# Kernel optimization log

Measured on AMD Instinct MI355X. Metric: run time of the kernel, lower is better.

Reference implementation:

```python
import jax, jax.numpy as jnp
import numpy as np

B, LQ, LF, NW, NFR, E, D, V = 4, 128, 64, 2, 8, 128, 128, 64


def _project(x, W, b):
    # torch Emb_Projection('linear'): Linear then zero-row mask
    y = x @ W + b
    m = 1.0 - jnp.all(y == 0, axis=-1, keepdims=True).astype(y.dtype)
    return y * m


def setup_inputs() -> dict:
    key = jax.random.key(0)
    ks = jax.random.split(key, 12)
    s = lambda k, shape, fan: jax.random.normal(k, shape, jnp.float32) / np.sqrt(fan)
    return {
        "query": jax.random.normal(ks[0], (B, LQ, E), jnp.float32),
        "fragment": jax.random.normal(ks[1], (B, NW, NFR, LF, E), jnp.float32),
        "query_mask": jnp.ones((B, LQ), jnp.float32),
        "fragment_mask": jnp.ones((B, NW, NFR, LF), jnp.float32),
        # learned params (stored [in, out]; torch Linear is x @ W.T with W [out,in])
        "proj_W": s(ks[2], (E, D), E),
        "proj_b": jnp.zeros((D,), jnp.float32),
        "self_att_W": s(ks[3], (NW, D), D),   # n_way Linear(D,1,bias=False)
        "q_att_W": s(ks[4], (D, V), D),
        "f_att_W": s(ks[5], (D, V), D),
        "qf_att_W": s(ks[6], (D, V), D),
        "gate_w": s(ks[7], (V,), V),          # value_gate: Linear(V,1,bias=False)
        "val_w": s(ks[8], (V,), V),           # value_att:  Linear(V,1,bias=False)
    }


def reference(query, fragment, query_mask, fragment_mask, proj_W, proj_b,
              self_att_W, q_att_W, f_att_W, qf_att_W, gate_w, val_w):
    query = _project(query, proj_W, proj_b)          # [B,Lq,D]
    fragment = _project(fragment, proj_W, proj_b)    # [B,NW,NFR,Lf,D]

    # (1) fragment self-attention -> frag_code
    logits = jnp.einsum('bwfld,wd->bwfl', fragment, self_att_W)   # per-way Linear(D,1)
    e = jnp.exp(logits) * fragment_mask
    frag_self_att = e / (e.sum(-1, keepdims=True) + 1e-7)          # [B,NW,NFR,Lf]
    frag_code = (fragment * frag_self_att[..., None]).sum(-2)     # [B,NW,NFR,D]

    # (2) query-to-fragment attention
    frag_r = fragment.reshape(fragment.shape[0], -1, fragment.shape[-2], fragment.shape[-1])  # [B,NF,Lf,D]
    qr = query[:, None]                                            # [B,1,Lq,D]
    q_att = qr @ q_att_W                                           # [B,1,Lq,V]
    f_att = frag_r @ f_att_W                                       # [B,NF,Lf,V]
    # large broadcast product [B,NF,Lf,Lq,D] then project to V
    qf = (qr[:, :, None, :, :] * frag_r[:, :, :, None, :]) @ qf_att_W  # [B,NF,Lf,Lq,V]
    qf = q_att[:, :, None] + f_att[:, :, :, None] + qf
    qf = qf.max(axis=-3)                                           # max over Lf -> [B,NF,Lq,V]

    qf_gate = jax.nn.sigmoid(qf @ gate_w) * query_mask[:, None]    # [B,NF,Lq]
    e2 = jnp.exp(qf @ val_w) * query_mask[:, None]
    qf_norm = e2 / (e2.sum(-1, keepdims=True) + 1e-7)              # [B,NF,Lq]

    query_code = (qr * qf_norm[..., None]).sum(axis=2)             # [B,NF,D]
    query_code = query_code.reshape(frag_code.shape)               # [B,NW,NFR,D]
    return frag_code, query_code, frag_self_att, qf_gate, query
```

## Files before the change

kernel.cpp:

```cpp
#include <hip/hip_runtime.h>
#include <hip/hip_bf16.h>

#define B_   4
#define LQ_  128
#define LF_  64
#define NW_  2
#define NFR_ 8
#define E_   128
#define D_   128
#define V_   64
#define NWF_ (NW_*NFR_)
#define NROW_Q (B_*LQ_)
#define NROW_F (B_*NW_*NFR_*LF_)

using bf16 = __hip_bfloat16;
typedef unsigned short u16;
typedef unsigned int   u32;
typedef __attribute__((ext_vector_type(8))) short  bf16x8;
typedef __attribute__((ext_vector_type(4))) float  f32x4;
typedef __attribute__((ext_vector_type(4))) u32    u32x4;

#define WS_QP    0
#define WS_QATT  65536
#define WS_E2    98304
#define WS_FP16  106496
#define WS_W3T   368640
#define WS_WFT   372736
#define WS_PWT   376832
#define WS_QAT   385024

#define OUT_FRAGCODE  0
#define OUT_QUERYCODE 8192
#define OUT_SELFATT   16384
#define OUT_QFGATE    20480
#define OUT_QUERY     28672

__device__ __forceinline__ float us2f(u16 v) { return __uint_as_float((u32)v << 16); }
__device__ __forceinline__ float lo2f(u32 v) { return __uint_as_float(v << 16); }
__device__ __forceinline__ float hi2f(u32 v) { return __uint_as_float(v & 0xffff0000u); }
__device__ __forceinline__ u16 f2b_raw(float f) {
    u32 u = __float_as_uint(f);
    return (u16)((u + 0x7fffu + ((u >> 16) & 1u)) >> 16);
}
__device__ __forceinline__ u32 pk2(float hi, float lo) {
    return __builtin_amdgcn_perm(__float_as_uint(hi), __float_as_uint(lo), 0x07060302u);
}
template<bool BF> __device__ __forceinline__ float LD(const void* p, int i) {
    return BF ? us2f(((const u16*)p)[i]) : ((const float*)p)[i];
}
template<bool BF> __device__ __forceinline__ void ST(void* p, int i, float v) {
    if (BF) ((u16*)p)[i] = f2b_raw(v); else ((float*)p)[i] = v;
}
template<bool BF> __device__ __forceinline__ u16 LDB(const void* p, int i) {
    return BF ? ((const u16*)p)[i] : f2b_raw(((const float*)p)[i]);
}
__device__ __forceinline__ bool is_bf(const void* qmask) {
    return ((const u16*)qmask)[0] == 0x3F80u;
}

template<bool BF>
__device__ __forceinline__ void prep_body(const void* src, u16* dst, u16* stg, int N)
{
    int t = threadIdx.x;
    int st = N + 1, total = 128 * N;
    for (int i = t; i < total; i += 256)
        stg[(i / N) * st + (i % N)] = LDB<BF>(src, i);
    __syncthreads();
    for (int j = t; j < total; j += 256) {
        int n = j >> 7, k = j & 127;
        dst[n * 128 + k] = stg[k * st + n];
    }
}
__global__ __launch_bounds__(256) void k_prep(
    const void* projW, const void* qattW, const void* qfW, const void* fattW,
    const void* qmask, float* ws)
{
    __shared__ u16 stg[128 * 129];
    int bx = blockIdx.x;
    const void* src = (bx == 0) ? projW : (bx == 1) ? qattW : (bx == 2) ? qfW : fattW;
    u16* dst = (u16*)(ws + ((bx == 0) ? WS_PWT : (bx == 1) ? WS_QAT : (bx == 2) ? WS_W3T : WS_WFT));
    int N = (bx == 0) ? 128 : 64;
    if (is_bf(qmask)) prep_body<true >(src, dst, stg, N);
    else              prep_body<false>(src, dst, stg, N);
}

template<bool BF>
__device__ __forceinline__ void proj_body(
    const void* query, const void* fragment, const void* projB,
    float* ws, void* out, u16* s_y)
{
    int r = blockIdx.x, t = threadIdx.x;
    int lane = t & 63, wave = t >> 6, m = lane & 15, quad = lane >> 4;
    bool isq = (r >= 256);
    int base = isq ? (r - 256) * 16 : r * 16;
    const void* x = isq ? query : fragment;
    const u16* pwt = (const u16*)(ws + WS_PWT);

    bf16x8 af[4];
    #pragma unroll
    for (int kt = 0; kt < 4; ++kt) {
        int off = (base + m) * 128 + kt * 32 + quad * 8;
        if (BF) af[kt] = *(const bf16x8*)((const u16*)x + off);
        else {
            f32x4 a = *(const f32x4*)((const float*)x + off);
            f32x4 c = *(const f32x4*)((const float*)x + off + 4);
            u32x4 av;
            av.x = pk2(a.y, a.x); av.y = pk2(a.w, a.z);
            av.z = pk2(c.y, c.x); av.w = pk2(c.w, c.z);
            af[kt] = __builtin_bit_cast(bf16x8, av);
        }
    }
    int nt0 = wave * 2;
    f32x4 acc[2];
    #pragma unroll
    for (int i = 0; i < 2; ++i) {
        float bv = LD<BF>(projB, (nt0 + i) * 16 + m);
        acc[i] = (f32x4){bv, bv, bv, bv};
    }
    #pragma unroll
    for (int kt = 0; kt < 4; ++kt)
        #pragma unroll
        for (int i = 0; i < 2; ++i) {
            bf16x8 bfr = *(const bf16x8*)(pwt + ((nt0 + i) * 16 + m) * 128 + kt * 32 + quad * 8);
            acc[i] = __builtin_amdgcn_mfma_f32_16x16x32_bf16(af[kt], bfr, acc[i], 0, 0, 0);
        }
    if (!isq) {
        u16* fp16 = (u16*)(ws + WS_FP16);
        #pragma unroll
        for (int i = 0; i < 2; ++i)
            #pragma unroll
            for (int rr = 0; rr < 4; ++rr)
                fp16[(size_t)(base + quad * 4 + rr) * 128 + (nt0 + i) * 16 + m] = f2b_raw(acc[i][rr]);
    } else {
        #pragma unroll
        for (int i = 0; i < 2; ++i)
            #pragma unroll
            for (int rr = 0; rr < 4; ++rr) {
                int gr = base + quad * 4 + rr, col = (nt0 + i) * 16 + m;
                float v = acc[i][rr];
                ws[WS_QP + (size_t)gr * 128 + col] = v;
                ST<BF>(out, OUT_QUERY + gr * 128 + col, v);
                s_y[(quad * 4 + rr) * 132 + col] = f2b_raw(v);
            }
        __syncthreads();
        bf16x8 ay[4];
        #pragma unroll
        for (int kt = 0; kt < 4; ++kt)
            ay[kt] = *(const bf16x8*)&s_y[m * 132 + kt * 32 + quad * 8];
        const u16* qat = (const u16*)(ws + WS_QAT);
        f32x4 a2 = (f32x4){0.f, 0.f, 0.f, 0.f};
        #pragma unroll
        for (int kt = 0; kt < 4; ++kt) {
            bf16x8 b2 = *(const bf16x8*)(qat + (wave * 16 + m) * 128 + kt * 32 + quad * 8);
            a2 = __builtin_amdgcn_mfma_f32_16x16x32_bf16(ay[kt], b2, a2, 0, 0, 0);
        }
        #pragma unroll
        for (int rr = 0; rr < 4; ++rr)
            ws[WS_QATT + (size_t)(base + quad * 4 + rr) * 64 + wave * 16 + m] = a2[rr];
    }
}
__global__ __launch_bounds__(256) void k_proj(
    const void* query, const void* fragment, const void* projB, const void* qmask,
    float* ws, void* out)
{
    __shared__ u16 s_y[16 * 132];
    if (is_bf(qmask)) proj_body<true >(query, fragment, projB, ws, out, s_y);
    else              proj_body<false>(query, fragment, projB, ws, out, s_y);
}

template<bool BF>
__device__ __forceinline__ void qf_body(
    const void* saW, const void* fmask, const void* gatew, const void* valw,
    const void* qmask, float* ws, void* out, char* smem)
{
    u16*   s_fp  = (u16*)smem;
    u16*   s_fa  = (u16*)(smem + 16384);
    float* s_saw = (float*)(smem + 34816);
    float* s_att = (float*)(smem + 35328);
    float* s_tmp = (float*)(smem + 35584);

    int t = threadIdx.x, lane = t & 63, wave = t >> 6;
    int bwf = blockIdx.x >> 2, qt2 = blockIdx.x & 3;
    int b = bwf >> 4;
    int m = lane & 15, quad = lane >> 4;
    int lq = wave >> 1, qsub = wave & 1;
    int sk = (m & 7) << 3;

    {
        const u32* src = (const u32*)((const u16*)(ws + WS_FP16)) + (size_t)bwf * 4096;
        u32* d32 = (u32*)s_fp;
        #pragma unroll
        for (int k = 0; k < 16; ++k) {
            int i = t + 512 * k;
            int row = i >> 6, cp = i & 63;
            d32[row * 64 + (cp ^ ((row & 7) << 2))] = src[i];
        }
    }
    const u16* w3t = (const u16*)(ws + WS_W3T);
    bf16x8 w3f[4][4];
    #pragma unroll
    for (int vt = 0; vt < 4; ++vt)
        #pragma unroll
        for (int kt = 0; kt < 4; ++kt)
            w3f[vt][kt] = *(const bf16x8*)(w3t + (vt * 16 + m) * 128 + kt * 32 + quad * 8);
    __syncthreads();

    int lbase = lq * 16;
    if (qsub == 0) {
        const u16* wft = (const u16*)(ws + WS_WFT);
        bf16x8 afk[4];
        #pragma unroll
        for (int kt = 0; kt < 4; ++kt)
            afk[kt] = *(const bf16x8*)&s_fp[(lbase + m) * 128 + ((kt * 32 + quad * 8) ^ sk)];
        #pragma unroll
        for (int vt = 0; vt < 4; ++vt) {
            bf16x8 wf = *(const bf16x8*)(wft + (vt * 16 + m) * 128 + 0 * 32 + quad * 8);
            f32x4 a0 = (f32x4){0.f, 0.f, 0.f, 0.f};
            #pragma unroll
            for (int kt = 0; kt < 4; ++kt) {
                bf16x8 wk = *(const bf16x8*)(wft + (vt * 16 + m) * 128 + kt * 32 + quad * 8);
                a0 = __builtin_amdgcn_mfma_f32_16x16x32_bf16(afk[kt], wk, a0, 0, 0, 0);
                (void)wf;
            }
            #pragma unroll
            for (int r = 0; r < 4; ++r)
                s_fa[(lbase + quad * 4 + r) * 72 + vt * 16 + m] = f2b_raw(a0[r]);
        }
    }
    float qpreg[4][8];
    {
        const float* qprow = ws + WS_QP + (size_t)(b * LQ_ + qt2 * 32 + qsub * 16 + m) * 128;
        #pragma unroll
        for (int kt = 0; kt < 4; ++kt) {
            f32x4 x0 = *(const f32x4*)(qprow + kt * 32 + quad * 8);
            f32x4 x1 = *(const f32x4*)(qprow + kt * 32 + quad * 8 + 4);
            qpreg[kt][0] = x0.x; qpreg[kt][1] = x0.y; qpreg[kt][2] = x0.z; qpreg[kt][3] = x0.w;
            qpreg[kt][4] = x1.x; qpreg[kt][5] = x1.y; qpreg[kt][6] = x1.z; qpreg[kt][7] = x1.w;
        }
    }
    __syncthreads();

    float mx[4][4];
    #pragma unroll
    for (int vt = 0; vt < 4; ++vt)
        #pragma unroll
        for (int r = 0; r < 4; ++r) mx[vt][r] = -1e30f;

    u32x4 fvc[4], fvn[4];
    #pragma unroll
    for (int kt = 0; kt < 4; ++kt)
        fvc[kt] = *(const u32x4*)&s_fp[lbase * 128 + (kt * 32 + quad * 8)];
    #pragma unroll 2
    for (int li = 0; li < 16; ++li) {
        if (li < 15) {
            int l2 = lbase + li + 1;
            #pragma unroll
            for (int kt = 0; kt < 4; ++kt)
                fvn[kt] = *(const u32x4*)&s_fp[l2 * 128 + ((kt * 32 + quad * 8) ^ (((li + 1) & 7) << 3))];
        }
        int l = lbase + li;
        bf16x8 af[4];
        #pragma unroll
        for (int kt = 0; kt < 4; ++kt) {
            u32x4 fv = fvc[kt];
            u32x4 av;
            av.x = pk2(qpreg[kt][1] * hi2f(fv.x), qpreg[kt][0] * lo2f(fv.x));
            av.y = pk2(qpreg[kt][3] * hi2f(fv.y), qpreg[kt][2] * lo2f(fv.y));
            av.z = pk2(qpreg[kt][5] * hi2f(fv.z), qpreg[kt][4] * lo2f(fv.z));
            av.w = pk2(qpreg[kt][7] * hi2f(fv.w), qpreg[kt][6] * lo2f(fv.w));
            af[kt] = __builtin_bit_cast(bf16x8, av);
        }
        #pragma unroll
        for (int vt = 0; vt < 4; ++vt) {
            float fa = us2f(s_fa[l * 72 + vt * 16 + m]);
            f32x4 acc = (f32x4){fa, fa, fa, fa};
            #pragma unroll
            for (int kt = 0; kt < 4; ++kt)
                acc = __builtin_amdgcn_mfma_f32_16x16x32_bf16(af[kt], w3f[vt][kt], acc, 0, 0, 0);
            #pragma unroll
            for (int r = 0; r < 4; ++r) mx[vt][r] = fmaxf(mx[vt][r], acc[r]);
        }
        #pragma unroll
        for (int kt = 0; kt < 4; ++kt) fvc[kt] = fvn[kt];
    }
    __syncthreads();
    #pragma unroll
    for (int vt = 0; vt < 4; ++vt)
        #pragma unroll
        for (int r = 0; r < 4; ++r)
            s_fa[(lq * 32 + qsub * 16 + quad * 4 + r) * 72 + vt * 16 + m] = f2b_raw(mx[vt][r]);
    __syncthreads();

    {
        int q = t >> 4, vg = t & 15;
        int gq = qt2 * 32 + q;
        float gp = 0.f, ep = 0.f;
        #pragma unroll
        for (int jj = 0; jj < 4; ++jj) {
            int v = vg * 4 + jj;
            float mval = -1e30f;
            #pragma unroll
            for (int w = 0; w < 4; ++w)
                mval = fmaxf(mval, us2f(s_fa[(w * 32 + q) * 72 + v]));
            float qf = mval + ws[WS_QATT + (size_t)(b * LQ_ + gq) * 64 + v];
            gp += qf * LD<BF>(gatew, v);
            ep += qf * LD<BF>(valw, v);
        }
        #pragma unroll
        for (int off = 1; off <= 8; off <<= 1) {
            gp += __shfl_xor(gp, off, 64);
            ep += __shfl_xor(ep, off, 64);
        }
        if (vg == 0) {
            float qm = LD<BF>(qmask, b * LQ_ + gq);
            float g = (1.0f / (1.0f + expf(-gp))) * qm;
            ST<BF>(out, OUT_QFGATE + bwf * LQ_ + gq, g);
            ws[WS_E2 + bwf * LQ_ + gq] = expf(ep) * qm;
        }
    }

    if (qt2 == 0) {
        if (t < 128) s_saw[t] = LD<BF>(saW, ((bwf >> 3) & 1) * 128 + t);
        __syncthreads();
        int l = t >> 3, j8 = t & 7;
        int swz = (l & 7) << 3;
        float p = 0.f;
        #pragma unroll
        for (int seg = 0; seg < 2; ++seg) {
            int koff = j8 * 16 + seg * 8;
            u32x4 fv = *(const u32x4*)&s_fp[l * 128 + (koff ^ swz)];
            const float* swp = &s_saw[koff];
            p += lo2f(fv.x) * swp[0] + hi2f(fv.x) * swp[1]
               + lo2f(fv.y) * swp[2] + hi2f(fv.y) * swp[3]
               + lo2f(fv.z) * swp[4] + hi2f(fv.z) * swp[5]
               + lo2f(fv.w) * swp[6] + hi2f(fv.w) * swp[7];
        }
        p += __shfl_xor(p, 1, 64);
        p += __shfl_xor(p, 2, 64);
        p += __shfl_xor(p, 4, 64);
        if (j8 == 0) s_att[l] = expf(p) * LD<BF>(fmask, bwf * LF_ + l);
        __syncthreads();
        if (t < 64) {
            float e = s_att[t], s = e;
            #pragma unroll
            for (int off = 1; off <= 32; off <<= 1) s += __shfl_xor(s, off, 64);
            float nrm = e / (s + 1e-7f);
            s_att[t] = nrm;
            ST<BF>(out, OUT_SELFATT + bwf * LF_ + t, nrm);
        }
        __syncthreads();
        int d = t & 127, grp = t >> 7;
        float fc = 0.f;
        #pragma unroll
        for (int li2 = 0; li2 < 16; ++li2) {
            int l2 = grp * 16 + li2;
            fc += us2f(s_fp[l2 * 128 + (d ^ ((l2 & 7) << 3))]) * s_att[l2];
        }
        s_tmp[grp * 128 + d] = fc;
        __syncthreads();
        if (t < 128)
            ST<BF>(out, OUT_FRAGCODE + bwf * D_ + t,
                   s_tmp[t] + s_tmp[128 + t] + s_tmp[256 + t] + s_tmp[384 + t]);
    }
}
__global__ __launch_bounds__(512) void k_qf(
    const void* saW, const void* fmask, const void* gatew, const void* valw,
    const void* qmask, float* ws, void* out)
{
    __shared__ char smem[37632];
    if (is_bf(qmask)) qf_body<true >(saW, fmask, gatew, valw, qmask, ws, out, smem);
    else              qf_body<false>(saW, fmask, gatew, valw, qmask, ws, out, smem);
}

template<bool BF>
__device__ __forceinline__ void qcode_body(const float* ws, void* out,
                                           float* s_n, float* s_part)
{
    int bwf = blockIdx.x, b = bwf >> 4, t = threadIdx.x;
    float e = ws[WS_E2 + bwf * LQ_ + t];
    float s = e;
    #pragma unroll
    for (int off = 1; off <= 32; off <<= 1) s += __shfl_xor(s, off, 64);
    if ((t & 63) == 0) s_part[t >> 6] = s;
    __syncthreads();
    float tot = s_part[0] + s_part[1] + 1e-7f;
    s_n[t] = e / tot;
    __syncthreads();
    float qc = 0.f;
    #pragma unroll 8
    for (int q = 0; q < LQ_; ++q)
        qc += ws[WS_QP + (size_t)(b * LQ_ + q) * 128 + t] * s_n[q];
    ST<BF>(out, OUT_QUERYCODE + bwf * D_ + t, qc);
}
__global__ __launch_bounds__(128) void k_qcode(const void* qmask, const float* ws, void* out)
{
    __shared__ float s_n[LQ_];
    __shared__ float s_part[2];
    if (is_bf(qmask)) qcode_body<true >(ws, out, s_n, s_part);
    else              qcode_body<false>(ws, out, s_n, s_part);
}

extern "C" void kernel_launch(void* const* d_in, const int* in_sizes, int n_in,
                              void* d_out, int out_size, void* d_ws, size_t ws_size,
                              hipStream_t stream)
{
    const void* query    = d_in[0];
    const void* fragment = d_in[1];
    const void* qmask    = d_in[2];
    const void* fmask    = d_in[3];
    const void* projW    = d_in[4];
    const void* projB    = d_in[5];
    const void* saW      = d_in[6];
    const void* qattW    = d_in[7];
    const void* fattW    = d_in[8];
    const void* qfW      = d_in[9];
    const void* gatew    = d_in[10];
    const void* valw     = d_in[11];
    float* ws = (float*)d_ws;

    hipLaunchKernelGGL(k_prep, dim3(4), dim3(256), 0, stream,
                       projW, qattW, qfW, fattW, qmask, ws);
    hipLaunchKernelGGL(k_proj, dim3(288), dim3(256), 0, stream,
                       query, fragment, projB, qmask, ws, d_out);
    hipLaunchKernelGGL(k_qf, dim3(256), dim3(512), 0, stream,
                       saW, fmask, gatew, valw, qmask, ws, d_out);
    hipLaunchKernelGGL(k_qcode, dim3(B_ * NWF_), dim3(128), 0, stream,
                       qmask, ws, d_out);
}
```

Baseline: 114.2 us.

## Fold weight prep into projection kernel and re-split qf work across more blocks

Removes the separate weight-transpose kernel. The projection kernel now reads projW and qattW directly with strided scalar loads, and two extra blocks transpose qfW and fattW. Projected fragments are written already swizzled so the qf kernel can copy them to shared memory linearly. The qf kernel goes from 256 blocks of 512 threads to 512 blocks of 256 threads. Each wave covers half of Lf and half of V, and partial maxima are combined in float through shared memory. The aim is to save a launch and improve occupancy and parallelism, at the cost of uncoalesced weight loads in k_proj and dropping the software prefetch in the max loop.

```diff
diff --git a/kernel.cpp b/kernel.cpp
--- a/kernel.cpp
+++ b/kernel.cpp
@@ -26,8 +26,6 @@
 #define WS_FP16  106496
 #define WS_W3T   368640
 #define WS_WFT   372736
-#define WS_PWT   376832
-#define WS_QAT   385024
 
 #define OUT_FRAGCODE  0
 #define OUT_QUERYCODE 8192
@@ -59,42 +57,34 @@
 }
 
 template<bool BF>
-__device__ __forceinline__ void prep_body(const void* src, u16* dst, u16* stg, int N)
-{
-    int t = threadIdx.x;
-    int st = N + 1, total = 128 * N;
-    for (int i = t; i < total; i += 256)
-        stg[(i / N) * st + (i % N)] = LDB<BF>(src, i);
-    __syncthreads();
-    for (int j = t; j < total; j += 256) {
-        int n = j >> 7, k = j & 127;
-        dst[n * 128 + k] = stg[k * st + n];
-    }
-}
-__global__ __launch_bounds__(256) void k_prep(
-    const void* projW, const void* qattW, const void* qfW, const void* fattW,
-    const void* qmask, float* ws)
-{
-    __shared__ u16 stg[128 * 129];
-    int bx = blockIdx.x;
-    const void* src = (bx == 0) ? projW : (bx == 1) ? qattW : (bx == 2) ? qfW : fattW;
-    u16* dst = (u16*)(ws + ((bx == 0) ? WS_PWT : (bx == 1) ? WS_QAT : (bx == 2) ? WS_W3T : WS_WFT));
-    int N = (bx == 0) ? 128 : 64;
-    if (is_bf(qmask)) prep_body<true >(src, dst, stg, N);
-    else              prep_body<false>(src, dst, stg, N);
-}
-
-template<bool BF>
 __device__ __forceinline__ void proj_body(
-    const void* query, const void* fragment, const void* projB,
-    float* ws, void* out, u16* s_y)
+    const void* query, const void* fragment, const void* projW, const void* projB,
+    const void* qattW, const void* qfW, const void* fattW,
+    float* ws, void* out, char* smem)
 {
     int r = blockIdx.x, t = threadIdx.x;
+    if (r >= 288) {
+        const void* src = (r == 288) ? qfW : fattW;
+        u16* dst = (u16*)(ws + ((r == 288) ? WS_W3T : WS_WFT));
+        u16* stg = (u16*)smem;
+        #pragma unroll
+        for (int it = 0; it < 32; ++it) {
+            int i = t + 256 * it;
+            stg[(i >> 6) * 65 + (i & 63)] = LDB<BF>(src, i);
+        }
+        __syncthreads();
+        #pragma unroll
+        for (int it = 0; it < 32; ++it) {
+            int j = t + 256 * it;
+            dst[(j >> 7) * 128 + (j & 127)] = stg[(j & 127) * 65 + (j >> 7)];
+        }
+        return;
+    }
+    u16* s_y = (u16*)smem;
     int lane = t & 63, wave = t >> 6, m = lane & 15, quad = lane >> 4;
     bool isq = (r >= 256);
     int base = isq ? (r - 256) * 16 : r * 16;
     const void* x = isq ? query : fragment;
-    const u16* pwt = (const u16*)(ws + WS_PWT);
 
     bf16x8 af[4];
     #pragma unroll
@@ -121,16 +111,26 @@
     for (int kt = 0; kt < 4; ++kt)
         #pragma unroll
         for (int i = 0; i < 2; ++i) {
-            bf16x8 bfr = *(const bf16x8*)(pwt + ((nt0 + i) * 16 + m) * 128 + kt * 32 + quad * 8);
+            int n = (nt0 + i) * 16 + m, k0 = kt * 32 + quad * 8;
+            short tmp[8];
+            #pragma unroll
+            for (int j = 0; j < 8; ++j)
+                tmp[j] = (short)LDB<BF>(projW, (k0 + j) * 128 + n);
+            bf16x8 bfr;
+            #pragma unroll
+            for (int j = 0; j < 8; ++j) bfr[j] = tmp[j];
             acc[i] = __builtin_amdgcn_mfma_f32_16x16x32_bf16(af[kt], bfr, acc[i], 0, 0, 0);
         }
     if (!isq) {
-        u16* fp16 = (u16*)(ws + WS_FP16);
+        u16* fp16 = (u16*)(ws + WS_FP16) + (size_t)(r >> 2) * 8192;
         #pragma unroll
         for (int i = 0; i < 2; ++i)
             #pragma unroll
-            for (int rr = 0; rr < 4; ++rr)
-                fp16[(size_t)(base + quad * 4 + rr) * 128 + (nt0 + i) * 16 + m] = f2b_raw(acc[i][rr]);
+            for (int rr = 0; rr < 4; ++rr) {
+                int row = (r & 3) * 16 + quad * 4 + rr;
+                int col = (nt0 + i) * 16 + m;
+                fp16[row * 128 + (col ^ ((row & 7) << 3))] = f2b_raw(acc[i][rr]);
+            }
     } else {
         #pragma unroll
         for (int i = 0; i < 2; ++i)
@@ -147,11 +147,17 @@
         #pragma unroll
         for (int kt = 0; kt < 4; ++kt)
             ay[kt] = *(const bf16x8*)&s_y[m * 132 + kt * 32 + quad * 8];
-        const u16* qat = (const u16*)(ws + WS_QAT);
         f32x4 a2 = (f32x4){0.f, 0.f, 0.f, 0.f};
         #pragma unroll
         for (int kt = 0; kt < 4; ++kt) {
-            bf16x8 b2 = *(const bf16x8*)(qat + (wave * 16 + m) * 128 + kt * 32 + quad * 8);
+            int v = wave * 16 + m, k0 = kt * 32 + quad * 8;
+            short tmp[8];
+            #pragma unroll
+            for (int j = 0; j < 8; ++j)
+                tmp[j] = (short)LDB<BF>(qattW, (k0 + j) * 64 + v);
+            bf16x8 b2;
+            #pragma unroll
+            for (int j = 0; j < 8; ++j) b2[j] = tmp[j];
             a2 = __builtin_amdgcn_mfma_f32_16x16x32_bf16(ay[kt], b2, a2, 0, 0, 0);
         }
         #pragma unroll
@@ -160,12 +166,13 @@
     }
 }
 __global__ __launch_bounds__(256) void k_proj(
-    const void* query, const void* fragment, const void* projB, const void* qmask,
+    const void* query, const void* fragment, const void* projW, const void* projB,
+    const void* qattW, const void* qfW, const void* fattW, const void* qmask,
     float* ws, void* out)
 {
-    __shared__ u16 s_y[16 * 132];
-    if (is_bf(qmask)) proj_body<true >(query, fragment, projB, ws, out, s_y);
-    else              proj_body<false>(query, fragment, projB, ws, out, s_y);
+    __shared__ char smem[16640];
+    if (is_bf(qmask)) proj_body<true >(query, fragment, projW, projB, qattW, qfW, fattW, ws, out, smem);
+    else              proj_body<false>(query, fragment, projW, projB, qattW, qfW, fattW, ws, out, smem);
 }
 
 template<bool BF>
@@ -173,63 +180,50 @@
     const void* saW, const void* fmask, const void* gatew, const void* valw,
     const void* qmask, float* ws, void* out, char* smem)
 {
-    u16*   s_fp  = (u16*)smem;
-    u16*   s_fa  = (u16*)(smem + 16384);
-    float* s_saw = (float*)(smem + 34816);
-    float* s_att = (float*)(smem + 35328);
-    float* s_tmp = (float*)(smem + 35584);
+    u16*   s_fp   = (u16*)smem;
+    u16*   s_fa   = (u16*)(smem + 16384);
+    float* s_pmax = (float*)(smem + 25600);
+    float* s_saw  = (float*)(smem + 34304);
+    float* s_att  = (float*)(smem + 34816);
+    float* s_tmp  = (float*)(smem + 35072);
 
     int t = threadIdx.x, lane = t & 63, wave = t >> 6;
-    int bwf = blockIdx.x >> 2, qt2 = blockIdx.x & 3;
+    int bwf = blockIdx.x >> 3, qt = blockIdx.x & 7;
     int b = bwf >> 4;
     int m = lane & 15, quad = lane >> 4;
-    int lq = wave >> 1, qsub = wave & 1;
-    int sk = (m & 7) << 3;
+    int lhalf = wave >> 1, vhalf = wave & 1;
 
     {
-        const u32* src = (const u32*)((const u16*)(ws + WS_FP16)) + (size_t)bwf * 4096;
+        const u32* src = (const u32*)((const u16*)(ws + WS_FP16) + (size_t)bwf * 8192);
         u32* d32 = (u32*)s_fp;
         #pragma unroll
-        for (int k = 0; k < 16; ++k) {
-            int i = t + 512 * k;
-            int row = i >> 6, cp = i & 63;
-            d32[row * 64 + (cp ^ ((row & 7) << 2))] = src[i];
-        }
-    }
-    const u16* w3t = (const u16*)(ws + WS_W3T);
-    bf16x8 w3f[4][4];
-    #pragma unroll
-    for (int vt = 0; vt < 4; ++vt)
-        #pragma unroll
-        for (int kt = 0; kt < 4; ++kt)
-            w3f[vt][kt] = *(const bf16x8*)(w3t + (vt * 16 + m) * 128 + kt * 32 + quad * 8);
+        for (int k = 0; k < 16; ++k) d32[t + 256 * k] = src[t + 256 * k];
+    }
     __syncthreads();
 
-    int lbase = lq * 16;
-    if (qsub == 0) {
+    {
+        int lr = wave * 16;
         const u16* wft = (const u16*)(ws + WS_WFT);
         bf16x8 afk[4];
         #pragma unroll
         for (int kt = 0; kt < 4; ++kt)
-            afk[kt] = *(const bf16x8*)&s_fp[(lbase + m) * 128 + ((kt * 32 + quad * 8) ^ sk)];
+            afk[kt] = *(const bf16x8*)&s_fp[(lr + m) * 128 + ((kt * 32 + quad * 8) ^ ((m & 7) << 3))];
         #pragma unroll
         for (int vt = 0; vt < 4; ++vt) {
-            bf16x8 wf = *(const bf16x8*)(wft + (vt * 16 + m) * 128 + 0 * 32 + quad * 8);
             f32x4 a0 = (f32x4){0.f, 0.f, 0.f, 0.f};
             #pragma unroll
             for (int kt = 0; kt < 4; ++kt) {
                 bf16x8 wk = *(const bf16x8*)(wft + (vt * 16 + m) * 128 + kt * 32 + quad * 8);
                 a0 = __builtin_amdgcn_mfma_f32_16x16x32_bf16(afk[kt], wk, a0, 0, 0, 0);
-                (void)wf;
             }
             #pragma unroll
             for (int r = 0; r < 4; ++r)
-                s_fa[(lbase + quad * 4 + r) * 72 + vt * 16 + m] = f2b_raw(a0[r]);
+                s_fa[(lr + quad * 4 + r) * 72 + vt * 16 + m] = f2b_raw(a0[r]);
         }
     }
     float qpreg[4][8];
     {
-        const float* qprow = ws + WS_QP + (size_t)(b * LQ_ + qt2 * 32 + qsub * 16 + m) * 128;
+        const float* qprow = ws + WS_QP + (size_t)(b * LQ_ + qt * 16 + m) * 128;
         #pragma unroll
         for (int kt = 0; kt < 4; ++kt) {
             f32x4 x0 = *(const f32x4*)(qprow + kt * 32 + quad * 8);
@@ -238,31 +232,32 @@
             qpreg[kt][4] = x1.x; qpreg[kt][5] = x1.y; qpreg[kt][6] = x1.z; qpreg[kt][7] = x1.w;
         }
     }
+    bf16x8 w3f[2][4];
+    {
+        const u16* w3t = (const u16*)(ws + WS_W3T);
+        #pragma unroll
+        for (int i = 0; i < 2; ++i)
+            #pragma unroll
+            for (int kt = 0; kt < 4; ++kt)
+                w3f[i][kt] = *(const bf16x8*)(w3t + ((vhalf * 2 + i) * 16 + m) * 128 + kt * 32 + quad * 8);
+    }
     __syncthreads();
 
-    float mx[4][4];
-    #pragma unroll
-    for (int vt = 0; vt < 4; ++vt)
-        #pragma unroll
-        for (int r = 0; r < 4; ++r) mx[vt][r] = -1e30f;
-
-    u32x4 fvc[4], fvn[4];
-    #pragma unroll
-    for (int kt = 0; kt < 4; ++kt)
-        fvc[kt] = *(const u32x4*)&s_fp[lbase * 128 + (kt * 32 + quad * 8)];
+    float mx[2][4];
+    #pragma unroll
+    for (int i = 0; i < 2; ++i)
+        #pragma unroll
+        for (int r = 0; r < 4; ++r) mx[i][r] = -1e30f;
+
+    int lbase = lhalf * 32;
     #pragma unroll 2
-    for (int li = 0; li < 16; ++li) {
-        if (li < 15) {
-            int l2 = lbase + li + 1;
-            #pragma unroll
-            for (int kt = 0; kt < 4; ++kt)
-                fvn[kt] = *(const u32x4*)&s_fp[l2 * 128 + ((kt * 32 + quad * 8) ^ (((li + 1) & 7) << 3))];
-        }
+    for (int li = 0; li < 32; ++li) {
         int l = lbase + li;
+        int sw = (l & 7) << 3;
         bf16x8 af[4];
         #pragma unroll
         for (int kt = 0; kt < 4; ++kt) {
-            u32x4 fv = fvc[kt];
+            u32x4 fv = *(const u32x4*)&s_fp[l * 128 + ((kt * 32 + quad * 8) ^ sw)];
             u32x4 av;
             av.x = pk2(qpreg[kt][1] * hi2f(fv.x), qpreg[kt][0] * lo2f(fv.x));
             av.y = pk2(qpreg[kt][3] * hi2f(fv.y), qpreg[kt][2] * lo2f(fv.y));
@@ -271,37 +266,31 @@
             af[kt] = __builtin_bit_cast(bf16x8, av);
         }
         #pragma unroll
-        for (int vt = 0; vt < 4; ++vt) {
-            float fa = us2f(s_fa[l * 72 + vt * 16 + m]);
+        for (int i = 0; i < 2; ++i) {
+            float fa = us2f(s_fa[l * 72 + (vhalf * 2 + i) * 16 + m]);
             f32x4 acc = (f32x4){fa, fa, fa, fa};
             #pragma unroll
             for (int kt = 0; kt < 4; ++kt)
-                acc = __builtin_amdgcn_mfma_f32_16x16x32_bf16(af[kt], w3f[vt][kt], acc, 0, 0, 0);
-            #pragma unroll
-            for (int r = 0; r < 4; ++r) mx[vt][r] = fmaxf(mx[vt][r], acc[r]);
-        }
-        #pragma unroll
-        for (int kt = 0; kt < 4; ++kt) fvc[kt] = fvn[kt];
-    }
-    __syncthreads();
-    #pragma unroll
-    for (int vt = 0; vt < 4; ++vt)
+                acc = __builtin_amdgcn_mfma_f32_16x16x32_bf16(af[kt], w3f[i][kt], acc, 0, 0, 0);
+            #pragma unroll
+            for (int r = 0; r < 4; ++r) mx[i][r] = fmaxf(mx[i][r], acc[r]);
+        }
+    }
+    #pragma unroll
+    for (int i = 0; i < 2; ++i)
         #pragma unroll
         for (int r = 0; r < 4; ++r)
-            s_fa[(lq * 32 + qsub * 16 + quad * 4 + r) * 72 + vt * 16 + m] = f2b_raw(mx[vt][r]);
+            s_pmax[lhalf * 1088 + (quad * 4 + r) * 68 + (vhalf * 2 + i) * 16 + m] = mx[i][r];
     __syncthreads();
 
     {
         int q = t >> 4, vg = t & 15;
-        int gq = qt2 * 32 + q;
+        int gq = qt * 16 + q;
         float gp = 0.f, ep = 0.f;
         #pragma unroll
         for (int jj = 0; jj < 4; ++jj) {
             int v = vg * 4 + jj;
-            float mval = -1e30f;
-            #pragma unroll
-            for (int w = 0; w < 4; ++w)
-                mval = fmaxf(mval, us2f(s_fa[(w * 32 + q) * 72 + v]));
+            float mval = fmaxf(s_pmax[q * 68 + v], s_pmax[1088 + q * 68 + v]);
             float qf = mval + ws[WS_QATT + (size_t)(b * LQ_ + gq) * 64 + v];
             gp += qf * LD<BF>(gatew, v);
             ep += qf * LD<BF>(valw, v);
@@ -319,15 +308,15 @@
         }
     }
 
-    if (qt2 == 0) {
+    if (qt == 0) {
         if (t < 128) s_saw[t] = LD<BF>(saW, ((bwf >> 3) & 1) * 128 + t);
         __syncthreads();
-        int l = t >> 3, j8 = t & 7;
+        int l = t >> 2, j4 = t & 3;
         int swz = (l & 7) << 3;
         float p = 0.f;
         #pragma unroll
-        for (int seg = 0; seg < 2; ++seg) {
-            int koff = j8 * 16 + seg * 8;
+        for (int seg = 0; seg < 4; ++seg) {
+            int koff = j4 * 32 + seg * 8;
             u32x4 fv = *(const u32x4*)&s_fp[l * 128 + (koff ^ swz)];
             const float* swp = &s_saw[koff];
             p += lo2f(fv.x) * swp[0] + hi2f(fv.x) * swp[1]
@@ -337,8 +326,7 @@
         }
         p += __shfl_xor(p, 1, 64);
         p += __shfl_xor(p, 2, 64);
-        p += __shfl_xor(p, 4, 64);
-        if (j8 == 0) s_att[l] = expf(p) * LD<BF>(fmask, bwf * LF_ + l);
+        if (j4 == 0) s_att[l] = expf(p) * LD<BF>(fmask, bwf * LF_ + l);
         __syncthreads();
         if (t < 64) {
             float e = s_att[t], s = e;
@@ -349,25 +337,23 @@
             ST<BF>(out, OUT_SELFATT + bwf * LF_ + t, nrm);
         }
         __syncthreads();
-        int d = t & 127, grp = t >> 7;
+        int d = t & 127, half = t >> 7;
         float fc = 0.f;
         #pragma unroll
-        for (int li2 = 0; li2 < 16; ++li2) {
-            int l2 = grp * 16 + li2;
+        for (int li2 = 0; li2 < 32; ++li2) {
+            int l2 = half * 32 + li2;
             fc += us2f(s_fp[l2 * 128 + (d ^ ((l2 & 7) << 3))]) * s_att[l2];
         }
-        s_tmp[grp * 128 + d] = fc;
-        __syncthreads();
-        if (t < 128)
-            ST<BF>(out, OUT_FRAGCODE + bwf * D_ + t,
-                   s_tmp[t] + s_tmp[128 + t] + s_tmp[256 + t] + s_tmp[384 + t]);
-    }
-}
-__global__ __launch_bounds__(512) void k_qf(
+        if (half == 1) s_tmp[d] = fc;
+        __syncthreads();
+        if (half == 0) ST<BF>(out, OUT_FRAGCODE + bwf * D_ + d, fc + s_tmp[d]);
+    }
+}
+__global__ __launch_bounds__(256, 4) void k_qf(
     const void* saW, const void* fmask, const void* gatew, const void* valw,
     const void* qmask, float* ws, void* out)
 {
-    __shared__ char smem[37632];
+    __shared__ char smem[35584];
     if (is_bf(qmask)) qf_body<true >(saW, fmask, gatew, valw, qmask, ws, out, smem);
     else              qf_body<false>(saW, fmask, gatew, valw, qmask, ws, out, smem);
 }
@@ -418,11 +404,9 @@
     const void* valw     = d_in[11];
     float* ws = (float*)d_ws;
 
-    hipLaunchKernelGGL(k_prep, dim3(4), dim3(256), 0, stream,
-                       projW, qattW, qfW, fattW, qmask, ws);
-    hipLaunchKernelGGL(k_proj, dim3(288), dim3(256), 0, stream,
-                       query, fragment, projB, qmask, ws, d_out);
-    hipLaunchKernelGGL(k_qf, dim3(256), dim3(512), 0, stream,
+    hipLaunchKernelGGL(k_proj, dim3(290), dim3(256), 0, stream,
+                       query, fragment, projW, projB, qattW, qfW, fattW, qmask, ws, d_out);
+    hipLaunchKernelGGL(k_qf, dim3(512), dim3(256), 0, stream,
                        saW, fmask, gatew, valw, qmask, ws, d_out);
     hipLaunchKernelGGL(k_qcode, dim3(B_ * NWF_), dim3(128), 0, stream,
                        qmask, ws, d_out);
```

Result: no change. 113.7 us (-0.5%).
